# Performance work log

Hardware: AMD Instinct MI355X
Metric: run time of the kernel (lower is better)

The kernel has to match this reference:

```python
import jax, jax.numpy as jnp
import numpy as np

B, L, DIM = 4, 8192, 512
HEADS, WIN = 8, 256
HID = int(DIM * 4.0)
HEAD_DIM = DIM // HEADS
EPS = 1e-5


def _layernorm(x, g, b):
    m = jnp.mean(x, axis=-1, keepdims=True)
    v = jnp.mean(jnp.square(x - m), axis=-1, keepdims=True)
    return (x - m) * jax.lax.rsqrt(v + EPS) * g + b


def setup_inputs() -> dict:
    key = jax.random.key(0)
    ks = jax.random.split(key, 8)
    s = 0.02
    return {
        "x": jax.random.normal(ks[0], (B, L, DIM), jnp.float32),
        "norm1_g": jnp.ones((DIM,), jnp.float32),
        "norm1_b": jnp.zeros((DIM,), jnp.float32),
        "qkv_w": jax.random.normal(ks[1], (DIM, 3 * DIM), jnp.float32) * s,
        "qkv_b": jnp.zeros((3 * DIM,), jnp.float32),
        "rpb_table": jax.random.normal(ks[2], (2 * WIN - 1, HEADS), jnp.float32) * s,
        "proj_w": jax.random.normal(ks[3], (DIM, DIM), jnp.float32) * s,
        "proj_b": jnp.zeros((DIM,), jnp.float32),
        "norm2_g": jnp.ones((DIM,), jnp.float32),
        "norm2_b": jnp.zeros((DIM,), jnp.float32),
        "fc1_w": jax.random.normal(ks[4], (DIM, HID), jnp.float32) * s,
        "fc1_b": jnp.zeros((HID,), jnp.float32),
        "fc2_w": jax.random.normal(ks[5], (HID, DIM), jnp.float32) * s,
        "fc2_b": jnp.zeros((DIM,), jnp.float32),
    }


def reference(x, norm1_g, norm1_b, qkv_w, qkv_b, rpb_table, proj_w, proj_b,
              norm2_g, norm2_b, fc1_w, fc1_b, fc2_w, fc2_b):
    scale = HEAD_DIM ** -0.5
    nW = L // WIN
    BW = B * nW

    shortcut = x
    h = _layernorm(x, norm1_g, norm1_b)
    xw = h.reshape(BW, WIN, DIM)

    qkv = (xw @ qkv_w + qkv_b).reshape(BW, WIN, 3, HEADS, HEAD_DIM)
    q = jnp.moveaxis(qkv[:, :, 0], 1, 2) * scale  # (BW, H, W, d)
    k = jnp.moveaxis(qkv[:, :, 1], 1, 2)
    v = jnp.moveaxis(qkv[:, :, 2], 1, 2)

    attn = jnp.einsum('bhqd,bhkd->bhqk', q, k)
    # relative position bias gather: (W, W, H) -> (H, W, W)
    coords = jnp.arange(WIN)
    ridx = coords[:, None] - coords[None, :] + WIN - 1
    bias = rpb_table[ridx]  # (W, W, H)
    attn = attn + jnp.transpose(bias, (2, 0, 1))[None]
    attn = jax.nn.softmax(attn, axis=-1)

    out = jnp.einsum('bhqk,bhkd->bhqd', attn, v)  # (BW, H, W, d)
    out = jnp.moveaxis(out, 1, 2).reshape(BW, WIN, DIM)
    out = out @ proj_w + proj_b

    x = shortcut + out.reshape(B, L, DIM)
    # NOTE: norm2 output feeds BOTH the residual branch and the MLP (as in source)
    x = _layernorm(x, norm2_g, norm2_b)
    m = jax.nn.gelu(x @ fc1_w + fc1_b, approximate=False) @ fc2_w + fc2_b
    return x + m
```

## Files before the change

kernel.cpp:

```cpp
#include <hip/hip_runtime.h>
#include <hip/hip_bf16.h>
#include <math.h>
#include <stdint.h>


typedef __attribute__((ext_vector_type(8))) __bf16 bf16x8;
typedef __attribute__((ext_vector_type(4))) __bf16 bf16x4;
typedef __attribute__((ext_vector_type(4))) float  f32x4;

#define NTOK  32768
#define DIMC  512
#define HEADS 8
#define WIN   256
#define HD    64
#define HIDC  2048

__device__ __forceinline__ void gld16(const __bf16* g, __bf16* l)
{
    __builtin_amdgcn_global_load_lds(
        (const __attribute__((address_space(1))) void*)g,
        (__attribute__((address_space(3))) void*)l, 16, 0, 0);
}

#define DSR(dst, base, off) \
    asm volatile("ds_read_b128 %0, %1 offset:" off : "=v"(dst) : "v"(base))

template<int MODE, int OUTF>
__global__ __launch_bounds__(512, 2) void gemm256(
    const __bf16* __restrict__ A, int lda,
    const __bf16* __restrict__ Bt, int ldb,
    const float* __restrict__ bias,
    const void* __restrict__ res, int res_f32,
    void* __restrict__ C, int ldc, int K,
    int nM, int nN)
{
    __shared__ __bf16 lds[2][2][16384];
    const int tid  = threadIdx.x;
    const int wave = tid >> 6, lane = tid & 63;
    const int quad = lane >> 4, l16 = lane & 15;
    const int wm = wave >> 2, wn = wave & 3;

    const int id  = blockIdx.x;
    const int xcd = id & 7;
    const int lid = id >> 3;
    const int mq  = lid / nN;
    const int mt  = xcd * (nM >> 3) + mq;
    const int nt  = lid - mq * nN;
    const int m0 = mt * 256, n0 = nt * 256;

    int aoff[4], boff[4];
    #pragma unroll
    for (int j = 0; j < 4; j++) {
        const int S = wave * 4 + j;
        const int row = (S >> 1) * 16 + l16;
        const int kof = (S & 1) * 32 + quad * 8;
        aoff[j] = (m0 + row) * lda + kof;
        boff[j] = (n0 + row) * ldb + kof;
    }

    const uint32_t lds0 =
        (uint32_t)(uintptr_t)(__attribute__((address_space(3))) void*)&lds[0][0][0];
    const uint32_t aAd0 = lds0 + wm * 16384 + lane * 16;
    const uint32_t bAd0 = lds0 + 32768 + wn * 8192 + lane * 16;

    f32x4 acc[8][4] = {};
    bf16x8 rA[4][2], rB[4][2];

    const int ntk = K >> 6;

    #pragma unroll
    for (int j = 0; j < 4; j++) {
        gld16(A  + aoff[j], &lds[0][0][(wave * 4 + j) * 512]);
        gld16(Bt + boff[j], &lds[0][1][(wave * 4 + j) * 512]);
    }
    #pragma unroll
    for (int j = 0; j < 4; j++) {
        gld16(A  + aoff[j] + 64, &lds[1][0][(wave * 4 + j) * 512]);
        gld16(Bt + boff[j] + 64, &lds[1][1][(wave * 4 + j) * 512]);
    }
    asm volatile("s_waitcnt vmcnt(8)");
    __builtin_amdgcn_s_barrier();

    for (int t = 0; t < ntk; ++t) {
        const int buf = t & 1;
        const uint32_t aAd = aAd0 + buf * 65536;
        const uint32_t bAd = bAd0 + buf * 65536;
        const bool pf = (t + 2 < ntk);
        const int kn = (t + 2) << 6;

        DSR(rA[0][0], aAd, "0");    DSR(rA[0][1], aAd, "1024");
        DSR(rA[1][0], aAd, "2048"); DSR(rA[1][1], aAd, "3072");
        DSR(rA[2][0], aAd, "4096"); DSR(rA[2][1], aAd, "5120");
        DSR(rA[3][0], aAd, "6144"); DSR(rA[3][1], aAd, "7168");
        DSR(rB[0][0], bAd, "0");    DSR(rB[0][1], bAd, "1024");
        DSR(rB[1][0], bAd, "2048"); DSR(rB[1][1], bAd, "3072");
        __builtin_amdgcn_s_barrier();
        asm volatile("s_waitcnt lgkmcnt(0)");
        __builtin_amdgcn_sched_barrier(0);
        __builtin_amdgcn_s_setprio(1);
        #pragma unroll
        for (int i = 0; i < 4; i++)
            #pragma unroll
            for (int j = 0; j < 2; j++)
                #pragma unroll
                for (int ks = 0; ks < 2; ks++)
                    acc[i][j] = __builtin_amdgcn_mfma_f32_16x16x32_bf16(
                        rB[j][ks], rA[i][ks], acc[i][j], 0, 0, 0);
        __builtin_amdgcn_s_setprio(0);
        __builtin_amdgcn_s_barrier();

        DSR(rB[2][0], bAd, "4096"); DSR(rB[2][1], bAd, "5120");
        DSR(rB[3][0], bAd, "6144"); DSR(rB[3][1], bAd, "7168");
        __builtin_amdgcn_s_barrier();
        asm volatile("s_waitcnt lgkmcnt(0)");
        __builtin_amdgcn_sched_barrier(0);
        __builtin_amdgcn_s_setprio(1);
        #pragma unroll
        for (int i = 0; i < 4; i++)
            #pragma unroll
            for (int j = 2; j < 4; j++)
                #pragma unroll
                for (int ks = 0; ks < 2; ks++)
                    acc[i][j] = __builtin_amdgcn_mfma_f32_16x16x32_bf16(
                        rB[j][ks], rA[i][ks], acc[i][j], 0, 0, 0);
        __builtin_amdgcn_s_setprio(0);
        __builtin_amdgcn_s_barrier();

        DSR(rA[0][0], aAd, "8192");  DSR(rA[0][1], aAd, "9216");
        DSR(rA[1][0], aAd, "10240"); DSR(rA[1][1], aAd, "11264");
        DSR(rA[2][0], aAd, "12288"); DSR(rA[2][1], aAd, "13312");
        DSR(rA[3][0], aAd, "14336"); DSR(rA[3][1], aAd, "15360");
        if (pf) {
            #pragma unroll
            for (int j = 0; j < 4; j++)
                gld16(Bt + boff[j] + kn, &lds[buf][1][(wave * 4 + j) * 512]);
        }
        __builtin_amdgcn_s_barrier();
        asm volatile("s_waitcnt lgkmcnt(0)");
        __builtin_amdgcn_sched_barrier(0);
        __builtin_amdgcn_s_setprio(1);
        #pragma unroll
        for (int i = 0; i < 4; i++)
            #pragma unroll
            for (int j = 0; j < 2; j++)
                #pragma unroll
                for (int ks = 0; ks < 2; ks++)
                    acc[4 + i][j] = __builtin_amdgcn_mfma_f32_16x16x32_bf16(
                        rB[j][ks], rA[i][ks], acc[4 + i][j], 0, 0, 0);
        __builtin_amdgcn_s_setprio(0);
        __builtin_amdgcn_s_barrier();

        if (pf) {
            #pragma unroll
            for (int j = 0; j < 4; j++)
                gld16(A + aoff[j] + kn, &lds[buf][0][(wave * 4 + j) * 512]);
        }
        __builtin_amdgcn_s_setprio(1);
        #pragma unroll
        for (int i = 0; i < 4; i++)
            #pragma unroll
            for (int j = 2; j < 4; j++)
                #pragma unroll
                for (int ks = 0; ks < 2; ks++)
                    acc[4 + i][j] = __builtin_amdgcn_mfma_f32_16x16x32_bf16(
                        rB[j][ks], rA[i][ks], acc[4 + i][j], 0, 0, 0);
        __builtin_amdgcn_s_setprio(0);
        if (pf)                  asm volatile("s_waitcnt vmcnt(8)");
        else if (t + 1 < ntk)    asm volatile("s_waitcnt vmcnt(0)");
        __builtin_amdgcn_s_barrier();
    }

    #pragma unroll
    for (int i = 0; i < 8; i++) {
        const int row = m0 + wm * 128 + i * 16 + l16;
        #pragma unroll
        for (int j = 0; j < 4; j++) {
            const int colb = n0 + wn * 64 + j * 16 + quad * 4;
            const size_t off = (size_t)row * ldc + colb;
            const f32x4 bv = *(const f32x4*)(bias + colb);
            f32x4 v;
            #pragma unroll
            for (int r = 0; r < 4; r++) v[r] = acc[i][j][r] + bv[r];
            if (MODE == 2) {
                #pragma unroll
                for (int r = 0; r < 4; r++)
                    v[r] = 0.5f * v[r] * (1.0f + erff(v[r] * 0.70710678118654752f));
            }
            if (MODE == 1) {
                if (res_f32) {
                    const f32x4 rv = *(const f32x4*)((const float*)res + off);
                    #pragma unroll
                    for (int r = 0; r < 4; r++) v[r] += rv[r];
                } else {
                    const bf16x4 rv = *(const bf16x4*)((const __bf16*)res + off);
                    #pragma unroll
                    for (int r = 0; r < 4; r++) v[r] += (float)rv[r];
                }
            }
            if (OUTF) {
                *(f32x4*)((float*)C + off) = v;
            } else {
                bf16x4 o;
                #pragma unroll
                for (int r = 0; r < 4; r++) o[r] = (__bf16)v[r];
                *(bf16x4*)((__bf16*)C + off) = o;
            }
        }
    }
}

__global__ __launch_bounds__(256) void attn_fused(
    const __bf16* __restrict__ qkvb, const float* __restrict__ rpb,
    const __bf16* __restrict__ Vt, __bf16* __restrict__ attnO)
{
    __shared__ __align__(16) __bf16 Qs[64 * 72];
    __shared__ __align__(16) __bf16 Ks[256 * 72];
    __shared__ float rpbs[320];
    const int bh = blockIdx.y;
    const int bw = bh >> 3, head = bh & 7;
    const int m0 = blockIdx.x * 64;
    const int tid = threadIdx.x;
    const __bf16* qb = qkvb + (size_t)bw * WIN * 1536 + head * HD;

    {
        const int row = tid >> 3, l8 = (tid & 7) * 8;
        #pragma unroll
        for (int p = 0; p < 2; p++) {
            const int r = p * 32 + row;
            *(bf16x8*)(Qs + r * 72 + l8) =
                *(const bf16x8*)(qb + (size_t)(m0 + r) * 1536 + l8);
        }
        #pragma unroll
        for (int p = 0; p < 8; p++) {
            const int r = p * 32 + row;
            *(bf16x8*)(Ks + r * 72 + l8) =
                *(const bf16x8*)(qb + 512 + (size_t)r * 1536 + l8);
        }
        rpbs[tid] = rpb[(size_t)(m0 + tid) * HEADS + head];
        if (tid < 63) rpbs[256 + tid] = rpb[(size_t)(m0 + 256 + tid) * HEADS + head];
    }
    __syncthreads();

    const int wave = tid >> 6, lane = tid & 63;
    const int quad = lane >> 4, l16 = lane & 15;
    bf16x8 af[2];
    #pragma unroll
    for (int ks = 0; ks < 2; ks++)
        af[ks] = *(const bf16x8*)(Qs + (wave * 16 + l16) * 72 + ks * 32 + quad * 8);

    f32x4 acc[16];
    #pragma unroll
    for (int nb = 0; nb < 16; nb++) acc[nb] = (f32x4){0.f, 0.f, 0.f, 0.f};
    #pragma unroll
    for (int nb = 0; nb < 16; nb++) {
        #pragma unroll
        for (int ks = 0; ks < 2; ks++) {
            bf16x8 bf = *(const bf16x8*)(Ks + (nb * 16 + l16) * 72 + ks * 32 + quad * 8);
            acc[nb] = __builtin_amdgcn_mfma_f32_16x16x32_bf16(af[ks], bf, acc[nb], 0, 0, 0);
        }
    }
    #pragma unroll
    for (int nb = 0; nb < 16; nb++)
        #pragma unroll
        for (int r = 0; r < 4; r++) {
            const int li = wave * 16 + quad * 4 + r;
            acc[nb][r] = acc[nb][r] * 0.125f + rpbs[li - nb * 16 - l16 + 255];
        }

    __syncthreads();

    char* Pb = (char*)Ks;
    #pragma unroll
    for (int r = 0; r < 4; r++) {
        float m = -1e30f;
        #pragma unroll
        for (int nb = 0; nb < 16; nb++) m = fmaxf(m, acc[nb][r]);
        #pragma unroll
        for (int msk = 1; msk < 16; msk <<= 1) m = fmaxf(m, __shfl_xor(m, msk));
        float s = 0.f;
        #pragma unroll
        for (int nb = 0; nb < 16; nb++) { acc[nb][r] = __expf(acc[nb][r] - m); s += acc[nb][r]; }
        #pragma unroll
        for (int msk = 1; msk < 16; msk <<= 1) s += __shfl_xor(s, msk);
        const float inv = 1.0f / s;
        const int row = wave * 16 + quad * 4 + r;
        const int rx = row & 7;
        #pragma unroll
        for (int nb = 0; nb < 16; nb++) {
            const int c = nb * 2 + (l16 >> 3);
            *(__bf16*)(Pb + row * 512 + ((c ^ rx) << 4) + ((l16 & 7) << 1)) =
                (__bf16)(acc[nb][r] * inv);
        }
    }
    __syncthreads();

    const __bf16* Vtb = Vt + (size_t)bh * (HD * WIN);
    const int prow = wave * 16 + l16;
    const int px = prow & 7;
    f32x4 acc2[4] = {};
    #pragma unroll
    for (int ks2 = 0; ks2 < 8; ks2++) {
        const bf16x8 pa = *(const bf16x8*)(Pb + prow * 512
                                + (((ks2 * 4 + quad) ^ px) << 4));
        #pragma unroll
        for (int nb2 = 0; nb2 < 4; nb2++) {
            const bf16x8 vf = *(const bf16x8*)(Vtb + (size_t)(nb2 * 16 + l16) * WIN
                                + ks2 * 32 + quad * 8);
            acc2[nb2] = __builtin_amdgcn_mfma_f32_16x16x32_bf16(vf, pa, acc2[nb2], 0, 0, 0);
        }
    }
    {
        const int i = m0 + wave * 16 + l16;
        __bf16* ob = attnO + (size_t)(bw * WIN + i) * DIMC + head * HD;
        #pragma unroll
        for (int nb2 = 0; nb2 < 4; nb2++) {
            bf16x4 o;
            #pragma unroll
            for (int r = 0; r < 4; r++) o[r] = (__bf16)acc2[nb2][r];
            *(bf16x4*)(ob + nb2 * 16 + quad * 4) = o;
        }
    }
}

__global__ __launch_bounds__(256) void vtrans(
    const __bf16* __restrict__ qkvb, __bf16* __restrict__ Vt, int bh_base)
{
    __shared__ __align__(16) __bf16 s[WIN * 72];
    const int bh = bh_base + blockIdx.x;
    const int bw = bh >> 3, head = bh & 7;
    const int tid = threadIdx.x;
    const __bf16* V = qkvb + (size_t)bw * WIN * 1536 + 1024 + head * HD;
    #pragma unroll
    for (int it = 0; it < 8; it++) {
        int idx = it * 256 + tid;
        int j = idx >> 3;
        int d0 = (idx & 7) * 8;
        *(bf16x8*)(s + j * 72 + d0) = *(const bf16x8*)(V + (size_t)j * 1536 + d0);
    }
    __syncthreads();
    __bf16* out = Vt + (size_t)blockIdx.x * (HD * WIN);
    #pragma unroll
    for (int it = 0; it < 8; it++) {
        int idx = it * 256 + tid;
        int d  = idx >> 5;
        int j0 = (idx & 31) * 8;
        bf16x8 v;
        #pragma unroll
        for (int j = 0; j < 8; j++) v[j] = s[(j0 + j) * 72 + d];
        *(bf16x8*)(out + (size_t)d * WIN + j0) = v;
    }
}

__global__ __launch_bounds__(256) void ln_kernel(
    const void* X, int xf,
    const float* __restrict__ g, const float* __restrict__ b,
    __bf16* O)
{
    const int tok  = blockIdx.x * 4 + (threadIdx.x >> 6);
    const int lane = threadIdx.x & 63;
    const size_t base = (size_t)tok * DIMC + lane * 8;
    float v[8];
    if (xf) {
        const float* xp = (const float*)X + base;
        f32x4 a = *(const f32x4*)xp;
        f32x4 c = *(const f32x4*)(xp + 4);
        #pragma unroll
        for (int j = 0; j < 4; j++) { v[j] = a[j]; v[4 + j] = c[j]; }
    } else {
        bf16x8 xv = *(const bf16x8*)((const __bf16*)X + base);
        #pragma unroll
        for (int j = 0; j < 8; j++) v[j] = (float)xv[j];
    }
    float s = 0.f, s2 = 0.f;
    #pragma unroll
    for (int j = 0; j < 8; j++) { s += v[j]; s2 += v[j] * v[j]; }
    #pragma unroll
    for (int off = 32; off; off >>= 1) { s += __shfl_xor(s, off); s2 += __shfl_xor(s2, off); }
    const float mean = s * (1.0f / DIMC);
    const float var  = s2 * (1.0f / DIMC) - mean * mean;
    const float rstd = rsqrtf(var + 1e-5f);
    f32x4 ga = *(const f32x4*)(g + lane * 8);
    f32x4 gc = *(const f32x4*)(g + lane * 8 + 4);
    f32x4 ba = *(const f32x4*)(b + lane * 8);
    f32x4 bc = *(const f32x4*)(b + lane * 8 + 4);
    bf16x8 ov;
    #pragma unroll
    for (int j = 0; j < 4; j++) {
        ov[j]     = (__bf16)((v[j]     - mean) * rstd * ga[j] + ba[j]);
        ov[4 + j] = (__bf16)((v[4 + j] - mean) * rstd * gc[j] + bc[j]);
    }
    *(bf16x8*)(O + base) = ov;
}

__global__ __launch_bounds__(256) void wtrans(
    const float* __restrict__ W, __bf16* __restrict__ Wt, int K, int N)
{
    __shared__ __align__(16) __bf16 s[64 * 72];
    const int kb = blockIdx.y * 64, nb = blockIdx.x * 64;
    const int tid = threadIdx.x;
    #pragma unroll
    for (int it = 0; it < 2; it++) {
        int idx = it * 256 + tid;
        int lk = idx >> 3;
        int ln = (idx & 7) * 8;
        const float* wp = W + (size_t)(kb + lk) * N + nb + ln;
        f32x4 a = *(const f32x4*)wp;
        f32x4 c = *(const f32x4*)(wp + 4);
        bf16x8 v;
        #pragma unroll
        for (int j = 0; j < 4; j++) { v[j] = (__bf16)a[j]; v[4 + j] = (__bf16)c[j]; }
        *(bf16x8*)(s + lk * 72 + ln) = v;
    }
    __syncthreads();
    #pragma unroll
    for (int it = 0; it < 2; it++) {
        int idx = it * 256 + tid;
        int ln  = idx >> 3;
        int lkv = (idx & 7) * 8;
        bf16x8 v;
        #pragma unroll
        for (int j = 0; j < 8; j++) v[j] = s[(lkv + j) * 72 + ln];
        *(bf16x8*)(Wt + (size_t)(nb + ln) * K + kb + lkv) = v;
    }
}

extern "C" void kernel_launch(void* const* d_in, const int* in_sizes, int n_in,
                              void* d_out, int out_size, void* d_ws, size_t ws_size,
                              hipStream_t stream)
{
    const float* x      = (const float*)d_in[0];
    const float* n1g    = (const float*)d_in[1];
    const float* n1b    = (const float*)d_in[2];
    const float* qkv_w  = (const float*)d_in[3];
    const float* qkv_b  = (const float*)d_in[4];
    const float* rpb    = (const float*)d_in[5];
    const float* proj_w = (const float*)d_in[6];
    const float* proj_b = (const float*)d_in[7];
    const float* n2g    = (const float*)d_in[8];
    const float* n2b    = (const float*)d_in[9];
    const float* fc1_w  = (const float*)d_in[10];
    const float* fc1_b  = (const float*)d_in[11];
    const float* fc2_w  = (const float*)d_in[12];
    const float* fc2_b  = (const float*)d_in[13];
    float* out = (float*)d_out;

    char* ws = (char*)d_ws;
    __bf16* qkvb  = (__bf16*)(ws + 0);
    __bf16* hid   = (__bf16*)(ws + 0);
    __bf16* Vt    = (__bf16*)(ws + 100663296);
    __bf16* h     = (__bf16*)(ws + 134217728);
    __bf16* y     = h;
    __bf16* attnO = (__bf16*)(ws + 167772160);
    __bf16* wq_t  = (__bf16*)(ws + 209715200);
    __bf16* wp_t  = (__bf16*)(ws + 211288064);
    __bf16* w1_t  = (__bf16*)(ws + 211812352);
    __bf16* w2_t  = (__bf16*)(ws + 213909504);

    wtrans<<<dim3(1536 / 64, 512 / 64),  256, 0, stream>>>(qkv_w, wq_t, 512, 1536);
    wtrans<<<dim3(512 / 64,  512 / 64),  256, 0, stream>>>(proj_w, wp_t, 512, 512);
    wtrans<<<dim3(2048 / 64, 512 / 64),  256, 0, stream>>>(fc1_w, w1_t, 512, 2048);
    wtrans<<<dim3(512 / 64,  2048 / 64), 256, 0, stream>>>(fc2_w, w2_t, 2048, 512);

    ln_kernel<<<NTOK / 4, 256, 0, stream>>>(x, 1, n1g, n1b, h);

    gemm256<0, 0><<<768, 512, 0, stream>>>(
        h, DIMC, wq_t, DIMC, qkv_b, nullptr, 0, qkvb, 1536, DIMC, 128, 6);

    vtrans<<<1024, 256, 0, stream>>>(qkvb, Vt, 0);
    attn_fused<<<dim3(4, 1024), 256, 0, stream>>>(qkvb, rpb, Vt, attnO);

    gemm256<1, 0><<<256, 512, 0, stream>>>(
        attnO, DIMC, wp_t, DIMC, proj_b, x, 1, y, DIMC, DIMC, 128, 2);

    ln_kernel<<<NTOK / 4, 256, 0, stream>>>(y, 0, n2g, n2b, y);

    gemm256<2, 0><<<1024, 512, 0, stream>>>(
        y, DIMC, w1_t, DIMC, fc1_b, nullptr, 0, hid, HIDC, DIMC, 128, 8);

    gemm256<1, 1><<<256, 512, 0, stream>>>(
        hid, HIDC, w2_t, HIDC, fc2_b, y, 0, out, DIMC, HIDC, 128, 2);
}
```

Measured before the change: 640.7 us.

## Make QKV and FC1 GEMMs persistent with next-tile prefetch overlapping epilogue

The GEMM kernel becomes persistent: each block loops over tiles with a stride of 256 and issues the next tile's first two K-stage loads before running the current tile's bias/GELU and store epilogue. The QKV and FC1 launches shrink to 256 blocks. This aims to hide the epilogue and prologue latency behind the memory loads, at the cost of fewer resident blocks per CU and less scheduler-level overlap between blocks.

After: 803.3 us. +25.4%, slower.

```diff
diff --git a/kernel.cpp b/kernel.cpp
--- a/kernel.cpp
+++ b/kernel.cpp
@@ -40,22 +40,27 @@
     const int quad = lane >> 4, l16 = lane & 15;
     const int wm = wave >> 2, wn = wave & 3;
 
-    const int id  = blockIdx.x;
-    const int xcd = id & 7;
-    const int lid = id >> 3;
-    const int mq  = lid / nN;
-    const int mt  = xcd * (nM >> 3) + mq;
-    const int nt  = lid - mq * nN;
-    const int m0 = mt * 256, n0 = nt * 256;
-
+    const int nT = nM * nN;
+    int id = blockIdx.x;
+
+    int m0, n0;
     int aoff[4], boff[4];
-    #pragma unroll
-    for (int j = 0; j < 4; j++) {
-        const int S = wave * 4 + j;
-        const int row = (S >> 1) * 16 + l16;
-        const int kof = (S & 1) * 32 + quad * 8;
-        aoff[j] = (m0 + row) * lda + kof;
-        boff[j] = (n0 + row) * ldb + kof;
+    const int srow = ((wave * 4) >> 1) * 16 + l16;
+    {
+        const int xcd = id & 7;
+        const int lid = id >> 3;
+        const int mq  = lid / nN;
+        const int mt  = xcd * (nM >> 3) + mq;
+        const int nt  = lid - mq * nN;
+        m0 = mt * 256; n0 = nt * 256;
+        #pragma unroll
+        for (int j = 0; j < 4; j++) {
+            const int S = wave * 4 + j;
+            const int row = (S >> 1) * 16 + l16;
+            const int kof = (S & 1) * 32 + quad * 8;
+            aoff[j] = (m0 + row) * lda + kof;
+            boff[j] = (n0 + row) * ldb + kof;
+        }
     }
 
     const uint32_t lds0 =
@@ -81,132 +86,188 @@
     asm volatile("s_waitcnt vmcnt(8)");
     __builtin_amdgcn_s_barrier();
 
-    for (int t = 0; t < ntk; ++t) {
-        const int buf = t & 1;
-        const uint32_t aAd = aAd0 + buf * 65536;
-        const uint32_t bAd = bAd0 + buf * 65536;
-        const bool pf = (t + 2 < ntk);
-        const int kn = (t + 2) << 6;
-
-        DSR(rA[0][0], aAd, "0");    DSR(rA[0][1], aAd, "1024");
-        DSR(rA[1][0], aAd, "2048"); DSR(rA[1][1], aAd, "3072");
-        DSR(rA[2][0], aAd, "4096"); DSR(rA[2][1], aAd, "5120");
-        DSR(rA[3][0], aAd, "6144"); DSR(rA[3][1], aAd, "7168");
-        DSR(rB[0][0], bAd, "0");    DSR(rB[0][1], bAd, "1024");
-        DSR(rB[1][0], bAd, "2048"); DSR(rB[1][1], bAd, "3072");
-        __builtin_amdgcn_s_barrier();
-        asm volatile("s_waitcnt lgkmcnt(0)");
-        __builtin_amdgcn_sched_barrier(0);
-        __builtin_amdgcn_s_setprio(1);
-        #pragma unroll
-        for (int i = 0; i < 4; i++)
-            #pragma unroll
-            for (int j = 0; j < 2; j++)
-                #pragma unroll
-                for (int ks = 0; ks < 2; ks++)
-                    acc[i][j] = __builtin_amdgcn_mfma_f32_16x16x32_bf16(
-                        rB[j][ks], rA[i][ks], acc[i][j], 0, 0, 0);
-        __builtin_amdgcn_s_setprio(0);
-        __builtin_amdgcn_s_barrier();
-
-        DSR(rB[2][0], bAd, "4096"); DSR(rB[2][1], bAd, "5120");
-        DSR(rB[3][0], bAd, "6144"); DSR(rB[3][1], bAd, "7168");
-        __builtin_amdgcn_s_barrier();
-        asm volatile("s_waitcnt lgkmcnt(0)");
-        __builtin_amdgcn_sched_barrier(0);
-        __builtin_amdgcn_s_setprio(1);
-        #pragma unroll
-        for (int i = 0; i < 4; i++)
-            #pragma unroll
-            for (int j = 2; j < 4; j++)
-                #pragma unroll
-                for (int ks = 0; ks < 2; ks++)
-                    acc[i][j] = __builtin_amdgcn_mfma_f32_16x16x32_bf16(
-                        rB[j][ks], rA[i][ks], acc[i][j], 0, 0, 0);
-        __builtin_amdgcn_s_setprio(0);
-        __builtin_amdgcn_s_barrier();
-
-        DSR(rA[0][0], aAd, "8192");  DSR(rA[0][1], aAd, "9216");
-        DSR(rA[1][0], aAd, "10240"); DSR(rA[1][1], aAd, "11264");
-        DSR(rA[2][0], aAd, "12288"); DSR(rA[2][1], aAd, "13312");
-        DSR(rA[3][0], aAd, "14336"); DSR(rA[3][1], aAd, "15360");
-        if (pf) {
+    for (;;) {
+        for (int t = 0; t < ntk; ++t) {
+            const int buf = t & 1;
+            const uint32_t aAd = aAd0 + buf * 65536;
+            const uint32_t bAd = bAd0 + buf * 65536;
+            const bool pf = (t + 2 < ntk);
+            const int kn = (t + 2) << 6;
+
+            DSR(rA[0][0], aAd, "0");    DSR(rA[0][1], aAd, "1024");
+            DSR(rA[1][0], aAd, "2048"); DSR(rA[1][1], aAd, "3072");
+            DSR(rA[2][0], aAd, "4096"); DSR(rA[2][1], aAd, "5120");
+            DSR(rA[3][0], aAd, "6144"); DSR(rA[3][1], aAd, "7168");
+            DSR(rB[0][0], bAd, "0");    DSR(rB[0][1], bAd, "1024");
+            DSR(rB[1][0], bAd, "2048"); DSR(rB[1][1], bAd, "3072");
+            __builtin_amdgcn_s_barrier();
+            asm volatile("s_waitcnt lgkmcnt(0)");
+            __builtin_amdgcn_sched_barrier(0);
+            __builtin_amdgcn_s_setprio(1);
+            #pragma unroll
+            for (int i = 0; i < 4; i++)
+                #pragma unroll
+                for (int j = 0; j < 2; j++)
+                    #pragma unroll
+                    for (int ks = 0; ks < 2; ks++)
+                        acc[i][j] = __builtin_amdgcn_mfma_f32_16x16x32_bf16(
+                            rB[j][ks], rA[i][ks], acc[i][j], 0, 0, 0);
+            __builtin_amdgcn_s_setprio(0);
+            __builtin_amdgcn_s_barrier();
+
+            DSR(rB[2][0], bAd, "4096"); DSR(rB[2][1], bAd, "5120");
+            DSR(rB[3][0], bAd, "6144"); DSR(rB[3][1], bAd, "7168");
+            __builtin_amdgcn_s_barrier();
+            asm volatile("s_waitcnt lgkmcnt(0)");
+            __builtin_amdgcn_sched_barrier(0);
+            __builtin_amdgcn_s_setprio(1);
+            #pragma unroll
+            for (int i = 0; i < 4; i++)
+                #pragma unroll
+                for (int j = 2; j < 4; j++)
+                    #pragma unroll
+                    for (int ks = 0; ks < 2; ks++)
+                        acc[i][j] = __builtin_amdgcn_mfma_f32_16x16x32_bf16(
+                            rB[j][ks], rA[i][ks], acc[i][j], 0, 0, 0);
+            __builtin_amdgcn_s_setprio(0);
+            __builtin_amdgcn_s_barrier();
+
+            DSR(rA[0][0], aAd, "8192");  DSR(rA[0][1], aAd, "9216");
+            DSR(rA[1][0], aAd, "10240"); DSR(rA[1][1], aAd, "11264");
+            DSR(rA[2][0], aAd, "12288"); DSR(rA[2][1], aAd, "13312");
+            DSR(rA[3][0], aAd, "14336"); DSR(rA[3][1], aAd, "15360");
+            if (pf) {
+                #pragma unroll
+                for (int j = 0; j < 4; j++)
+                    gld16(Bt + boff[j] + kn, &lds[buf][1][(wave * 4 + j) * 512]);
+            }
+            __builtin_amdgcn_s_barrier();
+            asm volatile("s_waitcnt lgkmcnt(0)");
+            __builtin_amdgcn_sched_barrier(0);
+            __builtin_amdgcn_s_setprio(1);
+            #pragma unroll
+            for (int i = 0; i < 4; i++)
+                #pragma unroll
+                for (int j = 0; j < 2; j++)
+                    #pragma unroll
+                    for (int ks = 0; ks < 2; ks++)
+                        acc[4 + i][j] = __builtin_amdgcn_mfma_f32_16x16x32_bf16(
+                            rB[j][ks], rA[i][ks], acc[4 + i][j], 0, 0, 0);
+            __builtin_amdgcn_s_setprio(0);
+            __builtin_amdgcn_s_barrier();
+
+            if (pf) {
+                #pragma unroll
+                for (int j = 0; j < 4; j++)
+                    gld16(A + aoff[j] + kn, &lds[buf][0][(wave * 4 + j) * 512]);
+            }
+            __builtin_amdgcn_s_setprio(1);
+            #pragma unroll
+            for (int i = 0; i < 4; i++)
+                #pragma unroll
+                for (int j = 2; j < 4; j++)
+                    #pragma unroll
+                    for (int ks = 0; ks < 2; ks++)
+                        acc[4 + i][j] = __builtin_amdgcn_mfma_f32_16x16x32_bf16(
+                            rB[j][ks], rA[i][ks], acc[4 + i][j], 0, 0, 0);
+            __builtin_amdgcn_s_setprio(0);
+            if (pf)                  asm volatile("s_waitcnt vmcnt(8)");
+            else if (t + 1 < ntk)    asm volatile("s_waitcnt vmcnt(0)");
+            __builtin_amdgcn_s_barrier();
+        }
+
+        const int em0 = m0, en0 = n0;
+        const int nid = id + 256;
+        const bool more = nid < nT;
+        if (more) {
+            const int xcd = nid & 7;
+            const int lid = nid >> 3;
+            const int mq  = lid / nN;
+            const int mt  = xcd * (nM >> 3) + mq;
+            const int nt  = lid - mq * nN;
+            m0 = mt * 256; n0 = nt * 256;
+            #pragma unroll
+            for (int j = 0; j < 4; j++) {
+                const int S = wave * 4 + j;
+                const int row = (S >> 1) * 16 + l16;
+                const int kof = (S & 1) * 32 + quad * 8;
+                aoff[j] = (m0 + row) * lda + kof;
+                boff[j] = (n0 + row) * ldb + kof;
+            }
+            #pragma unroll
+            for (int j = 0; j < 4; j++) {
+                gld16(A  + aoff[j], &lds[0][0][(wave * 4 + j) * 512]);
+                gld16(Bt + boff[j], &lds[0][1][(wave * 4 + j) * 512]);
+            }
+            #pragma unroll
+            for (int j = 0; j < 4; j++) {
+                gld16(A  + aoff[j] + 64, &lds[1][0][(wave * 4 + j) * 512]);
+                gld16(Bt + boff[j] + 64, &lds[1][1][(wave * 4 + j) * 512]);
+            }
+        }
+
+        #pragma unroll
+        for (int i = 0; i < 8; i++) {
+            #pragma unroll
+            for (int j = 0; j < 4; j++) {
+                const int colb = en0 + wn * 64 + j * 16 + quad * 4;
+                const f32x4 bv = *(const f32x4*)(bias + colb);
+                f32x4 v;
+                #pragma unroll
+                for (int r = 0; r < 4; r++) v[r] = acc[i][j][r] + bv[r];
+                if (MODE == 2) {
+                    #pragma unroll
+                    for (int r = 0; r < 4; r++)
+                        v[r] = 0.5f * v[r] * (1.0f + erff(v[r] * 0.70710678118654752f));
+                }
+                acc[i][j] = v;
+            }
+        }
+
+        if (more) {
+            asm volatile("s_waitcnt vmcnt(0)");
+            __builtin_amdgcn_s_barrier();
+        }
+
+        #pragma unroll
+        for (int i = 0; i < 8; i++) {
+            const int row = em0 + wm * 128 + i * 16 + l16;
+            #pragma unroll
+            for (int j = 0; j < 4; j++) {
+                const int colb = en0 + wn * 64 + j * 16 + quad * 4;
+                const size_t off = (size_t)row * ldc + colb;
+                f32x4 v = acc[i][j];
+                if (MODE == 1) {
+                    if (res_f32) {
+                        const f32x4 rv = *(const f32x4*)((const float*)res + off);
+                        #pragma unroll
+                        for (int r = 0; r < 4; r++) v[r] += rv[r];
+                    } else {
+                        const bf16x4 rv = *(const bf16x4*)((const __bf16*)res + off);
+                        #pragma unroll
+                        for (int r = 0; r < 4; r++) v[r] += (float)rv[r];
+                    }
+                }
+                if (OUTF) {
+                    *(f32x4*)((float*)C + off) = v;
+                } else {
+                    bf16x4 o;
+                    #pragma unroll
+                    for (int r = 0; r < 4; r++) o[r] = (__bf16)v[r];
+                    *(bf16x4*)((__bf16*)C + off) = o;
+                }
+            }
+        }
+
+        if (!more) break;
+        id = nid;
+        #pragma unroll
+        for (int i = 0; i < 8; i++)
             #pragma unroll
             for (int j = 0; j < 4; j++)
-                gld16(Bt + boff[j] + kn, &lds[buf][1][(wave * 4 + j) * 512]);
-        }
-        __builtin_amdgcn_s_barrier();
-        asm volatile("s_waitcnt lgkmcnt(0)");
-        __builtin_amdgcn_sched_barrier(0);
-        __builtin_amdgcn_s_setprio(1);
-        #pragma unroll
-        for (int i = 0; i < 4; i++)
-            #pragma unroll
-            for (int j = 0; j < 2; j++)
-                #pragma unroll
-                for (int ks = 0; ks < 2; ks++)
-                    acc[4 + i][j] = __builtin_amdgcn_mfma_f32_16x16x32_bf16(
-                        rB[j][ks], rA[i][ks], acc[4 + i][j], 0, 0, 0);
-        __builtin_amdgcn_s_setprio(0);
-        __builtin_amdgcn_s_barrier();
-
-        if (pf) {
-            #pragma unroll
-            for (int j = 0; j < 4; j++)
-                gld16(A + aoff[j] + kn, &lds[buf][0][(wave * 4 + j) * 512]);
-        }
-        __builtin_amdgcn_s_setprio(1);
-        #pragma unroll
-        for (int i = 0; i < 4; i++)
-            #pragma unroll
-            for (int j = 2; j < 4; j++)
-                #pragma unroll
-                for (int ks = 0; ks < 2; ks++)
-                    acc[4 + i][j] = __builtin_amdgcn_mfma_f32_16x16x32_bf16(
-                        rB[j][ks], rA[i][ks], acc[4 + i][j], 0, 0, 0);
-        __builtin_amdgcn_s_setprio(0);
-        if (pf)                  asm volatile("s_waitcnt vmcnt(8)");
-        else if (t + 1 < ntk)    asm volatile("s_waitcnt vmcnt(0)");
-        __builtin_amdgcn_s_barrier();
-    }
-
-    #pragma unroll
-    for (int i = 0; i < 8; i++) {
-        const int row = m0 + wm * 128 + i * 16 + l16;
-        #pragma unroll
-        for (int j = 0; j < 4; j++) {
-            const int colb = n0 + wn * 64 + j * 16 + quad * 4;
-            const size_t off = (size_t)row * ldc + colb;
-            const f32x4 bv = *(const f32x4*)(bias + colb);
-            f32x4 v;
-            #pragma unroll
-            for (int r = 0; r < 4; r++) v[r] = acc[i][j][r] + bv[r];
-            if (MODE == 2) {
-                #pragma unroll
-                for (int r = 0; r < 4; r++)
-                    v[r] = 0.5f * v[r] * (1.0f + erff(v[r] * 0.70710678118654752f));
-            }
-            if (MODE == 1) {
-                if (res_f32) {
-                    const f32x4 rv = *(const f32x4*)((const float*)res + off);
-                    #pragma unroll
-                    for (int r = 0; r < 4; r++) v[r] += rv[r];
-                } else {
-                    const bf16x4 rv = *(const bf16x4*)((const __bf16*)res + off);
-                    #pragma unroll
-                    for (int r = 0; r < 4; r++) v[r] += (float)rv[r];
-                }
-            }
-            if (OUTF) {
-                *(f32x4*)((float*)C + off) = v;
-            } else {
-                bf16x4 o;
-                #pragma unroll
-                for (int r = 0; r < 4; r++) o[r] = (__bf16)v[r];
-                *(bf16x4*)((__bf16*)C + off) = o;
-            }
-        }
-    }
+                acc[i][j] = (f32x4){0.f, 0.f, 0.f, 0.f};
+    }
+    (void)srow;
 }
 
 __global__ __launch_bounds__(256) void attn_fused(
@@ -463,7 +524,7 @@
 
     ln_kernel<<<NTOK / 4, 256, 0, stream>>>(x, 1, n1g, n1b, h);
 
-    gemm256<0, 0><<<768, 512, 0, stream>>>(
+    gemm256<0, 0><<<256, 512, 0, stream>>>(
         h, DIMC, wq_t, DIMC, qkv_b, nullptr, 0, qkvb, 1536, DIMC, 128, 6);
 
     vtrans<<<1024, 256, 0, stream>>>(qkvb, Vt, 0);
@@ -474,7 +535,7 @@
 
     ln_kernel<<<NTOK / 4, 256, 0, stream>>>(y, 0, n2g, n2b, y);
 
-    gemm256<2, 0><<<1024, 512, 0, stream>>>(
+    gemm256<2, 0><<<256, 512, 0, stream>>>(
         y, DIMC, w1_t, DIMC, fc1_b, nullptr, 0, hid, HIDC, DIMC, 128, 8);
 
     gemm256<1, 1><<<256, 512, 0, stream>>>(
```

## Transpose QK^T MFMA so each lane owns a query row in attention

Applied to the files above, without the earlier changes.

The attention kernel swaps the MFMA operands so the score accumulator is transposed, with each lane holding keys for a single query row. Softmax max and sum then need only two cross-lane shuffles instead of four per row, and probabilities are written to LDS as 4-wide bf16 vectors instead of scalar stores. Q is loaded straight from global memory into registers, which removes the Qs LDS staging buffer. The cost is uncoalesced strided global loads for Q and a different LDS bank-access pattern for the bias lookup.

Result: no change. 634.0 us (median of 4 runs) (-1.0%).

```diff
diff --git a/kernel.cpp b/kernel.cpp
--- a/kernel.cpp
+++ b/kernel.cpp
@@ -213,7 +213,6 @@
     const __bf16* __restrict__ qkvb, const float* __restrict__ rpb,
     const __bf16* __restrict__ Vt, __bf16* __restrict__ attnO)
 {
-    __shared__ __align__(16) __bf16 Qs[64 * 72];
     __shared__ __align__(16) __bf16 Ks[256 * 72];
     __shared__ float rpbs[320];
     const int bh = blockIdx.y;
@@ -222,14 +221,17 @@
     const int tid = threadIdx.x;
     const __bf16* qb = qkvb + (size_t)bw * WIN * 1536 + head * HD;
 
+    const int wave = tid >> 6, lane = tid & 63;
+    const int quad = lane >> 4, l16 = lane & 15;
+
+    bf16x8 af[2];
+    #pragma unroll
+    for (int ks = 0; ks < 2; ks++)
+        af[ks] = *(const bf16x8*)(qb + (size_t)(m0 + wave * 16 + l16) * 1536
+                                  + ks * 32 + quad * 8);
+
     {
         const int row = tid >> 3, l8 = (tid & 7) * 8;
-        #pragma unroll
-        for (int p = 0; p < 2; p++) {
-            const int r = p * 32 + row;
-            *(bf16x8*)(Qs + r * 72 + l8) =
-                *(const bf16x8*)(qb + (size_t)(m0 + r) * 1536 + l8);
-        }
         #pragma unroll
         for (int p = 0; p < 8; p++) {
             const int r = p * 32 + row;
@@ -241,13 +243,6 @@
     }
     __syncthreads();
 
-    const int wave = tid >> 6, lane = tid & 63;
-    const int quad = lane >> 4, l16 = lane & 15;
-    bf16x8 af[2];
-    #pragma unroll
-    for (int ks = 0; ks < 2; ks++)
-        af[ks] = *(const bf16x8*)(Qs + (wave * 16 + l16) * 72 + ks * 32 + quad * 8);
-
     f32x4 acc[16];
     #pragma unroll
     for (int nb = 0; nb < 16; nb++) acc[nb] = (f32x4){0.f, 0.f, 0.f, 0.f};
@@ -256,40 +251,47 @@
         #pragma unroll
         for (int ks = 0; ks < 2; ks++) {
             bf16x8 bf = *(const bf16x8*)(Ks + (nb * 16 + l16) * 72 + ks * 32 + quad * 8);
-            acc[nb] = __builtin_amdgcn_mfma_f32_16x16x32_bf16(af[ks], bf, acc[nb], 0, 0, 0);
-        }
-    }
+            acc[nb] = __builtin_amdgcn_mfma_f32_16x16x32_bf16(bf, af[ks], acc[nb], 0, 0, 0);
+        }
+    }
+    const int ql = wave * 16 + l16;
     #pragma unroll
     for (int nb = 0; nb < 16; nb++)
         #pragma unroll
-        for (int r = 0; r < 4; r++) {
-            const int li = wave * 16 + quad * 4 + r;
-            acc[nb][r] = acc[nb][r] * 0.125f + rpbs[li - nb * 16 - l16 + 255];
-        }
+        for (int r = 0; r < 4; r++)
+            acc[nb][r] = acc[nb][r] * 0.125f
+                       + rpbs[ql - (nb * 16 + quad * 4 + r) + 255];
 
     __syncthreads();
 
     char* Pb = (char*)Ks;
-    #pragma unroll
-    for (int r = 0; r < 4; r++) {
+    {
         float m = -1e30f;
         #pragma unroll
-        for (int nb = 0; nb < 16; nb++) m = fmaxf(m, acc[nb][r]);
-        #pragma unroll
-        for (int msk = 1; msk < 16; msk <<= 1) m = fmaxf(m, __shfl_xor(m, msk));
+        for (int nb = 0; nb < 16; nb++)
+            #pragma unroll
+            for (int r = 0; r < 4; r++) m = fmaxf(m, acc[nb][r]);
+        m = fmaxf(m, __shfl_xor(m, 16));
+        m = fmaxf(m, __shfl_xor(m, 32));
         float s = 0.f;
         #pragma unroll
-        for (int nb = 0; nb < 16; nb++) { acc[nb][r] = __expf(acc[nb][r] - m); s += acc[nb][r]; }
-        #pragma unroll
-        for (int msk = 1; msk < 16; msk <<= 1) s += __shfl_xor(s, msk);
+        for (int nb = 0; nb < 16; nb++)
+            #pragma unroll
+            for (int r = 0; r < 4; r++) {
+                acc[nb][r] = __expf(acc[nb][r] - m);
+                s += acc[nb][r];
+            }
+        s += __shfl_xor(s, 16);
+        s += __shfl_xor(s, 32);
         const float inv = 1.0f / s;
-        const int row = wave * 16 + quad * 4 + r;
-        const int rx = row & 7;
+        const int rx = ql & 7;
         #pragma unroll
         for (int nb = 0; nb < 16; nb++) {
-            const int c = nb * 2 + (l16 >> 3);
-            *(__bf16*)(Pb + row * 512 + ((c ^ rx) << 4) + ((l16 & 7) << 1)) =
-                (__bf16)(acc[nb][r] * inv);
+            bf16x4 o;
+            #pragma unroll
+            for (int r = 0; r < 4; r++) o[r] = (__bf16)(acc[nb][r] * inv);
+            const int c = nb * 2 + (quad >> 1);
+            *(bf16x4*)(Pb + ql * 512 + ((c ^ rx) << 4) + ((quad & 1) << 3)) = o;
         }
     }
     __syncthreads();
```
